# Performance work log

Measured on AMD Instinct MI355X. Metric: run time of the kernel, lower is better.

The kernel has to match this reference:

```python
import jax, jax.numpy as jnp
import numpy as np

N_NODES = 2_000_000
E = 1_000_000
MEM = 32      # memory_dim
MSG = 32      # message_dim
EMB = 32      # embed_dim
EDGE = 2      # edge_dim


def _linear_params(key, out_dim, in_dim):
    kw, kb = jax.random.split(key)
    bound = 1.0 / np.sqrt(in_dim)
    W = jax.random.uniform(kw, (out_dim, in_dim), jnp.float32, -bound, bound)
    b = jax.random.uniform(kb, (out_dim,), jnp.float32, -bound, bound)
    return W, b


def setup_inputs() -> dict:
    key = jax.random.key(0)
    ks = jax.random.split(key, 16)
    inp = {}
    inp["src_ids"] = jax.random.randint(ks[0], (E,), 0, N_NODES)
    inp["dst_ids"] = jax.random.randint(ks[1], (E,), 0, N_NODES)
    inp["edge_feat"] = jax.random.normal(ks[2], (E, EDGE), jnp.float32)
    inp["delta_t"] = jax.random.uniform(ks[3], (E, 1), jnp.float32)
    # persistent node memory (torch init is zeros; use randn for a non-trivial baseline)
    inp["memory"] = jax.random.normal(ks[4], (N_NODES, MEM), jnp.float32) * 0.1
    # MessageFunction MLP: (2*MEM + EDGE + 1) -> MSG -> MSG
    inp["msg_W1"], inp["msg_b1"] = _linear_params(ks[5], MSG, 2 * MEM + EDGE + 1)
    inp["msg_W2"], inp["msg_b2"] = _linear_params(ks[6], MSG, MSG)
    # GRUCell(MSG, MEM): weight_ih [3*MEM, MSG], weight_hh [3*MEM, MEM]
    inp["gru_w_ih"], inp["gru_b_ih"] = _linear_params(ks[7], 3 * MEM, MSG)
    inp["gru_w_hh"], inp["gru_b_hh"] = _linear_params(ks[8], 3 * MEM, MEM)
    # MultiheadAttention with seq_len=1: only V and out projections affect output
    inp["attn_Wv"], inp["attn_bv"] = _linear_params(ks[9], MEM, MEM)
    inp["attn_Wo"], inp["attn_bo"] = _linear_params(ks[10], MEM, MEM)
    # TemporalEmbedding MLP: (MEM + EDGE) -> EMB -> EMB
    inp["emb_W1"], inp["emb_b1"] = _linear_params(ks[11], EMB, MEM + EDGE)
    inp["emb_W2"], inp["emb_b2"] = _linear_params(ks[12], EMB, EMB)
    # AnomalyClassifier: EMB -> 32 -> 1
    inp["cls_W1"], inp["cls_b1"] = _linear_params(ks[13], 32, EMB)
    inp["cls_W2"], inp["cls_b2"] = _linear_params(ks[14], 1, 32)
    return inp


def reference(src_ids, dst_ids, edge_feat, delta_t, memory,
              msg_W1, msg_b1, msg_W2, msg_b2,
              gru_w_ih, gru_w_hh, gru_b_ih, gru_b_hh,
              attn_Wv, attn_bv, attn_Wo, attn_bo,
              emb_W1, emb_b1, emb_W2, emb_b2,
              cls_W1, cls_b1, cls_W2, cls_b2):
    # gather per-node memory  [E, MEM]
    src_mem = memory[src_ids]
    dst_mem = memory[dst_ids]

    # MessageFunction: concat + 2-layer MLP
    x = jnp.concatenate([src_mem, dst_mem, edge_feat, delta_t], axis=-1)  # [E, 67]
    h = jax.nn.relu(x @ msg_W1.T + msg_b1)
    msg = h @ msg_W2.T + msg_b2  # [E, MSG]

    # GRUCell update on dst memory (torch gate order: r, z, n)
    gi = msg @ gru_w_ih.T + gru_b_ih      # [E, 3*MEM]
    gh = dst_mem @ gru_w_hh.T + gru_b_hh  # [E, 3*MEM]
    i_r, i_z, i_n = jnp.split(gi, 3, axis=-1)
    h_r, h_z, h_n = jnp.split(gh, 3, axis=-1)
    r = jax.nn.sigmoid(i_r + h_r)
    z = jax.nn.sigmoid(i_z + h_z)
    n = jnp.tanh(i_n + r * h_n)
    updated = (1.0 - z) * n + z * dst_mem  # [E, MEM]
    # scatter back into persistent buffer (detached in the torch module)
    new_memory = memory.at[dst_ids].set(jax.lax.stop_gradient(updated))

    # TemporalEmbedding: self-attention over a length-1 sequence. softmax of a
    # single score is exactly 1, so attn_out == out_proj(v_proj(dst_mem)).
    attn_out = (dst_mem @ attn_Wv.T + attn_bv) @ attn_Wo.T + attn_bo  # [E, MEM]
    e = jnp.concatenate([attn_out, edge_feat], axis=-1)  # [E, MEM+EDGE]
    embed = jax.nn.relu(e @ emb_W1.T + emb_b1) @ emb_W2.T + emb_b2  # [E, EMB]

    # AnomalyClassifier (dropout is identity at eval)
    logits = jax.nn.relu(embed @ cls_W1.T + cls_b1) @ cls_W2.T + cls_b2  # [E, 1]
    probs = jax.nn.sigmoid(logits).squeeze(-1)  # [E]
    return probs, new_memory
```

## Files before the change

kernel.cpp:

```cpp
#include <hip/hip_runtime.h>
#include <hip/hip_bf16.h>

typedef float  f32x4v __attribute__((ext_vector_type(4)));
typedef short  bf16x8 __attribute__((ext_vector_type(8)));

#define NFRAG   26
#define TB_F32  512
#define FRG_U16 (NFRAG*512)
#define SHARE_BYTES (TB_F32*4 + FRG_U16*2)
#define SHARE_U4 (SHARE_BYTES/16)
#define WC_OFF 7168

#define BLK 256
#define COPY_BLOCKS 256
#define EDGE_BLOCKS 768
#define GRID (COPY_BLOCKS + EDGE_BLOCKS)
#define EDGE_WAVES (EDGE_BLOCKS * 4)

#define MFMA(a,b,c) __builtin_amdgcn_mfma_f32_16x16x32_bf16(a,b,c,0,0,0)

__device__ __forceinline__ float sigf(float v) { return 1.0f / (1.0f + __expf(-v)); }
__device__ __forceinline__ float tanhf_fast(float v) {
    float a = fabsf(v);
    float t = __expf(-2.0f * a);
    float r = (1.0f - t) / (1.0f + t);
    return v < 0.0f ? -r : r;
}
__device__ __forceinline__ unsigned pk(float a, float b) {
    union { __hip_bfloat162 h; unsigned u; } c;
    c.h = __float22bfloat162_rn(make_float2(a, b));
    return c.u;
}

union FragU { uint4 u4; bf16x8 s8; unsigned u[4]; };

__device__ __forceinline__ bf16x8 ldfrag(const unsigned short* frg, int idx_u16) {
    FragU c; c.u4 = *(const uint4*)(frg + idx_u16); return c.s8;
}
__device__ __forceinline__ f32x4v tbl(const float* tb, int idx_f32) {
    return *(const f32x4v*)(tb + idx_f32);
}
__device__ __forceinline__ bf16x8 relayout_reg(f32x4v h0, f32x4v h1) {
    FragU c;
    c.u[0] = pk(h0[0], h0[1]); c.u[1] = pk(h0[2], h0[3]);
    c.u[2] = pk(h1[0], h1[1]); c.u[3] = pk(h1[2], h1[3]);
    return c.s8;
}

__global__ void winner_k(const int* __restrict__ dst_ids, int* __restrict__ winner, int E) {
    int e = blockIdx.x * 256 + threadIdx.x;
    if (e < E) atomicMax(winner + dst_ids[e], e + 1);
}

__global__ void prep_k(const float* __restrict__ msg_W1, const float* __restrict__ msg_b1,
                       const float* __restrict__ msg_W2, const float* __restrict__ msg_b2,
                       const float* __restrict__ w_ih, const float* __restrict__ b_ih,
                       const float* __restrict__ w_hh, const float* __restrict__ b_hh,
                       const float* __restrict__ Wv, const float* __restrict__ bv,
                       const float* __restrict__ Wo, const float* __restrict__ bo,
                       const float* __restrict__ emb_W1, const float* __restrict__ emb_b1,
                       const float* __restrict__ emb_W2, const float* __restrict__ emb_b2,
                       const float* __restrict__ cls_W1, const float* __restrict__ cls_b1,
                       const float* __restrict__ cls_W2, float* __restrict__ WSf) {
    int t = threadIdx.x;
    float* tb = WSf;
    unsigned short* frg = (unsigned short*)(WSf + TB_F32);
    float* WC = WSf + WC_OFF;
    if (t < 32) {
        int j = t;
        tb[0*32+j]  = msg_b1[j];
        tb[1*32+j]  = msg_W1[j*67+64];
        tb[2*32+j]  = msg_W1[j*67+65];
        tb[3*32+j]  = msg_W1[j*67+66];
        tb[4*32+j]  = msg_b2[j];
        tb[5*32+j]  = b_ih[32+j] + b_hh[32+j];
        tb[6*32+j]  = b_ih[j] + b_hh[j];
        tb[7*32+j]  = b_hh[64+j];
        tb[8*32+j]  = b_ih[64+j];
        float a = bo[j];
        for (int o = 0; o < 32; ++o) a += Wo[j*32+o] * bv[o];
        tb[9*32+j]  = a;
        tb[10*32+j] = emb_b1[j];
        tb[11*32+j] = emb_W1[j*34+32];
        tb[12*32+j] = emb_W1[j*34+33];
        tb[13*32+j] = emb_b2[j];
        tb[14*32+j] = cls_b1[j];
        tb[15*32+j] = cls_W2[j];
    }
    for (int i = t; i < 1024; i += 256) {
        int j = i >> 5, k = i & 31;
        float a = 0.0f;
        for (int o = 0; o < 32; ++o) a += Wo[j*32+o] * Wv[o*32+k];
        WC[i] = a;
    }
    __syncthreads();
    for (int idx = t; idx < NFRAG * 512; idx += 256) {
        int f = idx >> 9, l = (idx >> 3) & 63, i = idx & 7;
        int r = l & 15, kb = ((l >> 4) << 3) + i;
        const float* P; int j0 = 0, k0 = 0, ld = 32;
        bool mapped = false;
        switch (f) {
            case 0:  P = msg_W1; j0 = 0;  k0 = 0;  ld = 67; break;
            case 1:  P = msg_W1; j0 = 0;  k0 = 32; ld = 67; break;
            case 2:  P = msg_W1; j0 = 16; k0 = 0;  ld = 67; break;
            case 3:  P = msg_W1; j0 = 16; k0 = 32; ld = 67; break;
            case 4:  P = msg_W2; j0 = 0;  mapped = true; break;
            case 5:  P = msg_W2; j0 = 16; mapped = true; break;
            case 6:  P = w_ih;   j0 = 32; mapped = true; break;
            case 7:  P = w_hh;   j0 = 32; break;
            case 8:  P = w_ih;   j0 = 48; mapped = true; break;
            case 9:  P = w_hh;   j0 = 48; break;
            case 10: P = w_ih;   j0 = 0;  mapped = true; break;
            case 11: P = w_hh;   j0 = 0;  break;
            case 12: P = w_ih;   j0 = 16; mapped = true; break;
            case 13: P = w_hh;   j0 = 16; break;
            case 14: P = w_hh;   j0 = 64; break;
            case 15: P = w_hh;   j0 = 80; break;
            case 16: P = w_ih;   j0 = 64; mapped = true; break;
            case 17: P = w_ih;   j0 = 80; mapped = true; break;
            case 18: P = WC;     j0 = 0;  break;
            case 19: P = WC;     j0 = 16; break;
            case 20: P = emb_W1; j0 = 0;  ld = 34; mapped = true; break;
            case 21: P = emb_W1; j0 = 16; ld = 34; mapped = true; break;
            case 22: P = emb_W2; j0 = 0;  mapped = true; break;
            case 23: P = emb_W2; j0 = 16; mapped = true; break;
            case 24: P = cls_W1; j0 = 0;  mapped = true; break;
            default: P = cls_W1; j0 = 16; mapped = true; break;
        }
        int kidx = kb;
        if (mapped) kidx = 16 * ((kb >> 2) & 1) + 4 * (kb >> 3) + (kb & 3);
        __hip_bfloat16 hv = __float2bfloat16(P[(j0 + r) * ld + k0 + kidx]);
        frg[idx] = *(unsigned short*)&hv;
    }
}

__device__ __forceinline__ void compute16(
    int grp, int E, int eI, int g, int lane,
    int e, int dst, int winv, float2 ef, float dtv,
    f32x4v sa, f32x4v sb, f32x4v da, f32x4v db, f32x4v t0, f32x4v t1,
    const float* tb, const unsigned short* frg, float clsb2,
    float* __restrict__ probs, float* __restrict__ out_mem) {
    int ob = 0, tbo = 0;
    asm volatile("" : "+v"(ob), "+v"(tbo));

    FragU Bs, Bd;
    Bs.u[0] = pk(sa[0], sa[1]); Bs.u[1] = pk(sa[2], sa[3]);
    Bs.u[2] = pk(sb[0], sb[1]); Bs.u[3] = pk(sb[2], sb[3]);
    Bd.u[0] = pk(da[0], da[1]); Bd.u[1] = pk(da[2], da[3]);
    Bd.u[2] = pk(db[0], db[1]); Bd.u[3] = pk(db[2], db[3]);
    f32x4v dmt[2]; dmt[0] = t0; dmt[1] = t1;

    f32x4v h[2];
#pragma unroll
    for (int jt = 0; jt < 2; ++jt) {
        f32x4v b1v = tbl(tb, 0*32 + jt*16 + 4*g + tbo);
        f32x4v w64 = tbl(tb, 1*32 + jt*16 + 4*g + tbo);
        f32x4v w65 = tbl(tb, 2*32 + jt*16 + 4*g + tbo);
        f32x4v w66 = tbl(tb, 3*32 + jt*16 + 4*g + tbo);
        f32x4v c;
#pragma unroll
        for (int i = 0; i < 4; ++i)
            c[i] = b1v[i] + ef.x * w64[i] + ef.y * w65[i] + dtv * w66[i];
        c = MFMA(ldfrag(frg, (jt*2+1)*512 + lane*8 + ob), Bd.s8, c);
        c = MFMA(ldfrag(frg, (jt*2+0)*512 + lane*8 + ob), Bs.s8, c);
#pragma unroll
        for (int i = 0; i < 4; ++i) c[i] = fmaxf(c[i], 0.0f);
        h[jt] = c;
    }
    bf16x8 Bh = relayout_reg(h[0], h[1]);

    f32x4v m[2];
#pragma unroll
    for (int jt = 0; jt < 2; ++jt)
        m[jt] = MFMA(ldfrag(frg, (4+jt)*512 + lane*8 + ob), Bh,
                     tbl(tb, 4*32 + jt*16 + 4*g + tbo));
    bf16x8 Bm = relayout_reg(m[0], m[1]);

    f32x4v zz[2], uu[2];
#pragma unroll
    for (int jt = 0; jt < 2; ++jt) {
        f32x4v c = tbl(tb, 5*32 + jt*16 + 4*g + tbo);
        c = MFMA(ldfrag(frg, (7+2*jt)*512 + lane*8 + ob), Bd.s8, c);
        c = MFMA(ldfrag(frg, (6+2*jt)*512 + lane*8 + ob), Bm, c);
#pragma unroll
        for (int i = 0; i < 4; ++i) c[i] = sigf(c[i]);
        zz[jt] = c;
    }
#pragma unroll
    for (int jt = 0; jt < 2; ++jt) {
        f32x4v c = tbl(tb, 6*32 + jt*16 + 4*g + tbo);
        c = MFMA(ldfrag(frg, (11+2*jt)*512 + lane*8 + ob), Bd.s8, c);
        c = MFMA(ldfrag(frg, (10+2*jt)*512 + lane*8 + ob), Bm, c);
        f32x4v hn = tbl(tb, 7*32 + jt*16 + 4*g + tbo);
        hn = MFMA(ldfrag(frg, (14+jt)*512 + lane*8 + ob), Bd.s8, hn);
        f32x4v bin = tbl(tb, 8*32 + jt*16 + 4*g + tbo);
        f32x4v npre;
#pragma unroll
        for (int i = 0; i < 4; ++i) npre[i] = fmaf(sigf(c[i]), hn[i], bin[i]);
        npre = MFMA(ldfrag(frg, (16+jt)*512 + lane*8 + ob), Bm, npre);
#pragma unroll
        for (int i = 0; i < 4; ++i) {
            float n = tanhf_fast(npre[i]);
            uu[jt][i] = n + zz[jt][i] * (dmt[jt][i] - n);
        }
    }
    if (winv == e + 1) {
        f32x4v* orow = (f32x4v*)(out_mem + (size_t)dst * 32);
        orow[g]     = uu[0];
        orow[4 + g] = uu[1];
    }

    f32x4v at[2];
#pragma unroll
    for (int jt = 0; jt < 2; ++jt)
        at[jt] = MFMA(ldfrag(frg, (18+jt)*512 + lane*8 + ob), Bd.s8,
                      tbl(tb, 9*32 + jt*16 + 4*g + tbo));
    bf16x8 Ba = relayout_reg(at[0], at[1]);
    f32x4v e1v[2];
#pragma unroll
    for (int jt = 0; jt < 2; ++jt) {
        f32x4v b  = tbl(tb, 10*32 + jt*16 + 4*g + tbo);
        f32x4v wa = tbl(tb, 11*32 + jt*16 + 4*g + tbo);
        f32x4v wb = tbl(tb, 12*32 + jt*16 + 4*g + tbo);
        f32x4v c;
#pragma unroll
        for (int i = 0; i < 4; ++i) c[i] = b[i] + ef.x * wa[i] + ef.y * wb[i];
        c = MFMA(ldfrag(frg, (20+jt)*512 + lane*8 + ob), Ba, c);
#pragma unroll
        for (int i = 0; i < 4; ++i) c[i] = fmaxf(c[i], 0.0f);
        e1v[jt] = c;
    }
    bf16x8 B1 = relayout_reg(e1v[0], e1v[1]);
    f32x4v e2v[2];
#pragma unroll
    for (int jt = 0; jt < 2; ++jt)
        e2v[jt] = MFMA(ldfrag(frg, (22+jt)*512 + lane*8 + ob), B1,
                       tbl(tb, 13*32 + jt*16 + 4*g + tbo));
    bf16x8 B2 = relayout_reg(e2v[0], e2v[1]);
    float part = 0.0f;
#pragma unroll
    for (int jt = 0; jt < 2; ++jt) {
        f32x4v c = MFMA(ldfrag(frg, (24+jt)*512 + lane*8 + ob), B2,
                        tbl(tb, 14*32 + jt*16 + 4*g + tbo));
        f32x4v w2 = tbl(tb, 15*32 + jt*16 + 4*g + tbo);
#pragma unroll
        for (int i = 0; i < 4; ++i) part = fmaf(fmaxf(c[i], 0.0f), w2[i], part);
    }
    part += __shfl_xor(part, 16);
    part += __shfl_xor(part, 32);
    if (lane < 16) {
        int ee = grp * 16 + eI;
        if (ee < E) probs[ee] = sigf(part + clsb2);
    }
}

__global__ __launch_bounds__(BLK, 4) void tgn_mfma16(
    const int* __restrict__ src_ids, const int* __restrict__ dst_ids,
    const float* __restrict__ edge_feat, const float* __restrict__ delta_t,
    const float* __restrict__ memory, const float* __restrict__ cls_b2,
    const float* __restrict__ WSf, const int* __restrict__ winner,
    float* __restrict__ probs, float* __restrict__ out_mem,
    int E, int N, int ngrp) {
    __shared__ uint4 sbuf[SHARE_U4];
    int bid = blockIdx.x, tid = threadIdx.x;

    if (bid < COPY_BLOCKS) {
        const f32x4v* m4 = (const f32x4v*)memory;
        f32x4v* o4 = (f32x4v*)out_mem;
        const long S = (long)COPY_BLOCKS * BLK;
        const long total4 = (long)N * 8;
        long i0 = (long)bid * BLK + tid;
        for (; i0 + 3 * S < total4; i0 += 4 * S) {
            long i1 = i0 + S, i2 = i0 + 2 * S, i3 = i0 + 3 * S;
            int w0 = winner[i0 >> 3];
            int w1 = winner[i1 >> 3];
            int w2 = winner[i2 >> 3];
            int w3 = winner[i3 >> 3];
            if (w0 == 0) o4[i0] = m4[i0];
            if (w1 == 0) o4[i1] = m4[i1];
            if (w2 == 0) o4[i2] = m4[i2];
            if (w3 == 0) o4[i3] = m4[i3];
        }
        for (; i0 < total4; i0 += S) {
            if (winner[i0 >> 3] == 0) o4[i0] = m4[i0];
        }
        return;
    }

    {
        const uint4* s = (const uint4*)WSf;
        for (int i = tid; i < SHARE_U4; i += BLK) sbuf[i] = s[i];
    }
    __syncthreads();
    const float* tb = (const float*)sbuf;
    const unsigned short* frg = (const unsigned short*)((const float*)sbuf + TB_F32);
    int wv = tid >> 6, lane = tid & 63;
    int eI = lane & 15, g = lane >> 4;
    int ewid = (bid - COPY_BLOCKS) * 4 + wv;
    float clsb2 = cls_b2[0];

#define PREF(P, G) do {                                                              \
    int ee = (G) * 16 + eI; if (ee >= E) ee = E - 1;                                 \
    e##P = ee;                                                                       \
    int sid = src_ids[ee]; dst##P = dst_ids[ee];                                     \
    ef##P = ((const float2*)edge_feat)[ee]; dt##P = delta_t[ee];                     \
    win##P = winner[dst##P];                                                         \
    const f32x4v* sp_ = (const f32x4v*)(memory + (size_t)sid * 32);                  \
    const f32x4v* dp_ = (const f32x4v*)(memory + (size_t)dst##P * 32);               \
    S##P##a = sp_[2*g]; S##P##b = sp_[2*g+1];                                        \
    D##P##a = dp_[2*g]; D##P##b = dp_[2*g+1];                                        \
    T##P##0 = dp_[g];   T##P##1 = dp_[4+g];                                          \
} while (0)

#define PIN(P) asm volatile("" : "+v"(S##P##a), "+v"(S##P##b), "+v"(D##P##a),        \
                                 "+v"(D##P##b), "+v"(T##P##0), "+v"(T##P##1),        \
                                 "+v"(win##P), "+v"(dt##P))

    int g0 = ewid;
    if (g0 < ngrp) {
        int eA, dstA, winA; float2 efA; float dtA;
        f32x4v SAa, SAb, DAa, DAb, TA0, TA1;
        int eB, dstB, winB; float2 efB; float dtB;
        f32x4v SBa, SBb, DBa, DBb, TB0, TB1;
        PREF(A, g0);
        for (;;) {
            int gn = g0 + EDGE_WAVES;
            { int gp = (gn < ngrp) ? gn : (ngrp - 1); PREF(B, gp); PIN(B); }
            compute16(g0, E, eI, g, lane, eA, dstA, winA, efA, dtA,
                      SAa, SAb, DAa, DAb, TA0, TA1,
                      tb, frg, clsb2, probs, out_mem);
            if (gn >= ngrp) break;
            g0 = gn;
            gn = g0 + EDGE_WAVES;
            { int gp = (gn < ngrp) ? gn : (ngrp - 1); PREF(A, gp); PIN(A); }
            compute16(g0, E, eI, g, lane, eB, dstB, winB, efB, dtB,
                      SBa, SBb, DBa, DBb, TB0, TB1,
                      tb, frg, clsb2, probs, out_mem);
            if (gn >= ngrp) break;
            g0 = gn;
        }
    }
#undef PREF
#undef PIN
}

extern "C" void kernel_launch(void* const* d_in, const int* in_sizes, int n_in,
                              void* d_out, int out_size, void* d_ws, size_t ws_size,
                              hipStream_t stream) {
    const int*   src_ids   = (const int*)d_in[0];
    const int*   dst_ids   = (const int*)d_in[1];
    const float* edge_feat = (const float*)d_in[2];
    const float* delta_t   = (const float*)d_in[3];
    const float* memory    = (const float*)d_in[4];
    const float* msg_W1 = (const float*)d_in[5],  *msg_b1 = (const float*)d_in[6];
    const float* msg_W2 = (const float*)d_in[7],  *msg_b2 = (const float*)d_in[8];
    const float* w_ih   = (const float*)d_in[9],  *b_ih   = (const float*)d_in[10];
    const float* w_hh   = (const float*)d_in[11], *b_hh   = (const float*)d_in[12];
    const float* Wv     = (const float*)d_in[13], *bv     = (const float*)d_in[14];
    const float* Wo     = (const float*)d_in[15], *bo     = (const float*)d_in[16];
    const float* emb_W1 = (const float*)d_in[17], *emb_b1 = (const float*)d_in[18];
    const float* emb_W2 = (const float*)d_in[19], *emb_b2 = (const float*)d_in[20];
    const float* cls_W1 = (const float*)d_in[21], *cls_b1 = (const float*)d_in[22];
    const float* cls_W2 = (const float*)d_in[23], *cls_b2 = (const float*)d_in[24];

    int E = in_sizes[0];
    int N = in_sizes[4] / 32;
    int ngrp = (E + 15) / 16;

    int*   winner = (int*)d_ws;
    float* WSf    = (float*)((char*)d_ws + (size_t)N * sizeof(int));
    float* probs  = (float*)d_out;
    float* outmem = probs + E;

    hipMemsetAsync(winner, 0, (size_t)N * sizeof(int), stream);
    winner_k<<<(E + 255) / 256, 256, 0, stream>>>(dst_ids, winner, E);
    prep_k<<<1, 256, 0, stream>>>(msg_W1, msg_b1, msg_W2, msg_b2,
                                  w_ih, b_ih, w_hh, b_hh,
                                  Wv, bv, Wo, bo,
                                  emb_W1, emb_b1, emb_W2, emb_b2,
                                  cls_W1, cls_b1, cls_W2, WSf);
    tgn_mfma16<<<GRID, BLK, 0, stream>>>(src_ids, dst_ids, edge_feat, delta_t,
                                         memory, cls_b2, WSf, winner,
                                         probs, outmem, E, N, ngrp);
}
```

Measured before the change: 293.8 us.

## Software-pipeline edge gathers with inline-asm loads and branchless trash-buffer stores

Restructures the edge loop into a two-deep software pipeline. Edge ids and features for the next-next group are issued with inline-asm global loads, and the gathered memory rows for the next group are issued before the current group's compute. Explicit s_waitcnt vmcnt(3) points with sched barriers keep the compiler from serialising these loads, so gather latency can be hidden behind MFMA work. The conditional memory-row store is made branchless: losing edges write to a per-wave trash area in the workspace, which removes divergence but adds extra stores. Manual vmcnt accounting is fragile, because stores also count against vmcnt and the loads are opaque to the compiler.

```diff
diff --git a/kernel.cpp b/kernel.cpp
--- a/kernel.cpp
+++ b/kernel.cpp
@@ -2,6 +2,7 @@
 #include <hip/hip_bf16.h>
 
 typedef float  f32x4v __attribute__((ext_vector_type(4)));
+typedef float  f32x2v __attribute__((ext_vector_type(2)));
 typedef short  bf16x8 __attribute__((ext_vector_type(8)));
 
 #define NFRAG   26
@@ -136,10 +137,10 @@
 
 __device__ __forceinline__ void compute16(
     int grp, int E, int eI, int g, int lane,
-    int e, int dst, int winv, float2 ef, float dtv,
+    int e, int dst, int winv, f32x2v ef, float dtv,
     f32x4v sa, f32x4v sb, f32x4v da, f32x4v db, f32x4v t0, f32x4v t1,
     const float* tb, const unsigned short* frg, float clsb2,
-    float* __restrict__ probs, float* __restrict__ out_mem) {
+    float* __restrict__ probs, float* __restrict__ out_mem, float* trash) {
     int ob = 0, tbo = 0;
     asm volatile("" : "+v"(ob), "+v"(tbo));
 
@@ -160,7 +161,7 @@
         f32x4v c;
 #pragma unroll
         for (int i = 0; i < 4; ++i)
-            c[i] = b1v[i] + ef.x * w64[i] + ef.y * w65[i] + dtv * w66[i];
+            c[i] = b1v[i] + ef[0] * w64[i] + ef[1] * w65[i] + dtv * w66[i];
         c = MFMA(ldfrag(frg, (jt*2+1)*512 + lane*8 + ob), Bd.s8, c);
         c = MFMA(ldfrag(frg, (jt*2+0)*512 + lane*8 + ob), Bs.s8, c);
 #pragma unroll
@@ -204,10 +205,14 @@
             uu[jt][i] = n + zz[jt][i] * (dmt[jt][i] - n);
         }
     }
-    if (winv == e + 1) {
+    {
+        bool w = (winv == e + 1);
         f32x4v* orow = (f32x4v*)(out_mem + (size_t)dst * 32);
-        orow[g]     = uu[0];
-        orow[4 + g] = uu[1];
+        f32x4v* tr   = (f32x4v*)trash;
+        f32x4v* p0 = w ? orow + g     : tr + g;
+        f32x4v* p1 = w ? orow + 4 + g : tr + 4 + g;
+        *p0 = uu[0];
+        *p1 = uu[1];
     }
 
     f32x4v at[2];
@@ -224,7 +229,7 @@
         f32x4v wb = tbl(tb, 12*32 + jt*16 + 4*g + tbo);
         f32x4v c;
 #pragma unroll
-        for (int i = 0; i < 4; ++i) c[i] = b[i] + ef.x * wa[i] + ef.y * wb[i];
+        for (int i = 0; i < 4; ++i) c[i] = b[i] + ef[0] * wa[i] + ef[1] * wb[i];
         c = MFMA(ldfrag(frg, (20+jt)*512 + lane*8 + ob), Ba, c);
 #pragma unroll
         for (int i = 0; i < 4; ++i) c[i] = fmaxf(c[i], 0.0f);
@@ -259,7 +264,7 @@
     const float* __restrict__ edge_feat, const float* __restrict__ delta_t,
     const float* __restrict__ memory, const float* __restrict__ cls_b2,
     const float* __restrict__ WSf, const int* __restrict__ winner,
-    float* __restrict__ probs, float* __restrict__ out_mem,
+    float* __restrict__ probs, float* __restrict__ out_mem, float* trashbase,
     int E, int N, int ngrp) {
     __shared__ uint4 sbuf[SHARE_U4];
     int bid = blockIdx.x, tid = threadIdx.x;
@@ -298,50 +303,100 @@
     int eI = lane & 15, g = lane >> 4;
     int ewid = (bid - COPY_BLOCKS) * 4 + wv;
     float clsb2 = cls_b2[0];
-
-#define PREF(P, G) do {                                                              \
-    int ee = (G) * 16 + eI; if (ee >= E) ee = E - 1;                                 \
-    e##P = ee;                                                                       \
-    int sid = src_ids[ee]; dst##P = dst_ids[ee];                                     \
-    ef##P = ((const float2*)edge_feat)[ee]; dt##P = delta_t[ee];                     \
-    win##P = winner[dst##P];                                                         \
-    const f32x4v* sp_ = (const f32x4v*)(memory + (size_t)sid * 32);                  \
-    const f32x4v* dp_ = (const f32x4v*)(memory + (size_t)dst##P * 32);               \
-    S##P##a = sp_[2*g]; S##P##b = sp_[2*g+1];                                        \
-    D##P##a = dp_[2*g]; D##P##b = dp_[2*g+1];                                        \
-    T##P##0 = dp_[g];   T##P##1 = dp_[4+g];                                          \
+    float* trash = trashbase + (((bid - COPY_BLOCKS) * 4 + wv) & 31) * 32;
+
+#define IDS_ASM(P, G) do {                                                           \
+    int ee_ = (G) * 16 + eI; if (ee_ >= E) ee_ = E - 1;                              \
+    e##P = ee_;                                                                      \
+    asm volatile("global_load_dword %0, %1, off"                                     \
+                 : "=v"(sid##P) : "v"((unsigned long long)(src_ids + ee_)));         \
+    asm volatile("global_load_dword %0, %1, off"                                     \
+                 : "=v"(dst##P) : "v"((unsigned long long)(dst_ids + ee_)));         \
+    asm volatile("global_load_dwordx2 %0, %1, off"                                   \
+                 : "=v"(ef##P) : "v"((unsigned long long)(edge_feat + 2*(size_t)ee_)));\
+    asm volatile("global_load_dword %0, %1, off"                                     \
+                 : "=v"(dt##P) : "v"((unsigned long long)(delta_t + ee_)));          \
 } while (0)
 
-#define PIN(P) asm volatile("" : "+v"(S##P##a), "+v"(S##P##b), "+v"(D##P##a),        \
-                                 "+v"(D##P##b), "+v"(T##P##0), "+v"(T##P##1),        \
-                                 "+v"(win##P), "+v"(dt##P))
-
-    int g0 = ewid;
-    if (g0 < ngrp) {
-        int eA, dstA, winA; float2 efA; float dtA;
+#define ROWS_ASM(P) do {                                                             \
+    unsigned long long sb_ = (unsigned long long)(memory + (size_t)sid##P * 32);     \
+    unsigned long long db_ = (unsigned long long)(memory + (size_t)dst##P * 32);     \
+    asm volatile("global_load_dwordx4 %0, %1, off" : "=v"(S##P##a) : "v"(sb_ + 32ull*g));      \
+    asm volatile("global_load_dwordx4 %0, %1, off" : "=v"(S##P##b) : "v"(sb_ + 32ull*g + 16)); \
+    asm volatile("global_load_dwordx4 %0, %1, off" : "=v"(D##P##a) : "v"(db_ + 32ull*g));      \
+    asm volatile("global_load_dwordx4 %0, %1, off" : "=v"(D##P##b) : "v"(db_ + 32ull*g + 16)); \
+    asm volatile("global_load_dwordx4 %0, %1, off" : "=v"(T##P##0) : "v"(db_ + 16ull*g));      \
+    asm volatile("global_load_dwordx4 %0, %1, off" : "=v"(T##P##1) : "v"(db_ + 64 + 16ull*g)); \
+    asm volatile("global_load_dword %0, %1, off"                                     \
+                 : "=v"(win##P) : "v"((unsigned long long)(winner + dst##P)));       \
+} while (0)
+
+#define WAITPF(Q, P) do {                                                            \
+    asm volatile("s_waitcnt vmcnt(3)"                                                \
+        : "+v"(S##Q##a), "+v"(S##Q##b), "+v"(D##Q##a), "+v"(D##Q##b),                \
+          "+v"(T##Q##0), "+v"(T##Q##1), "+v"(win##Q),                                \
+          "+v"(sid##P), "+v"(dst##P), "+v"(ef##P), "+v"(dt##P) :: "memory");         \
+    __builtin_amdgcn_sched_barrier(0);                                               \
+} while (0)
+
+    int gA = ewid, gB = ewid + EDGE_WAVES;
+    if (gA < ngrp) {
+        int eA, sidA, dstA, winA; f32x2v efA; float dtA;
         f32x4v SAa, SAb, DAa, DAb, TA0, TA1;
-        int eB, dstB, winB; float2 efB; float dtB;
+        int eB, sidB, dstB, winB; f32x2v efB; float dtB;
         f32x4v SBa, SBb, DBa, DBb, TB0, TB1;
-        PREF(A, g0);
+
+        {
+            int ee = gA * 16 + eI; if (ee >= E) ee = E - 1;
+            eA = ee;
+            sidA = src_ids[ee]; dstA = dst_ids[ee];
+            efA = ((const f32x2v*)edge_feat)[ee]; dtA = delta_t[ee];
+            winA = winner[dstA];
+            const f32x4v* sp_ = (const f32x4v*)memory + (size_t)sidA * 8;
+            const f32x4v* dp_ = (const f32x4v*)memory + (size_t)dstA * 8;
+            SAa = sp_[2*g]; SAb = sp_[2*g+1];
+            DAa = dp_[2*g]; DAb = dp_[2*g+1];
+            TA0 = dp_[g];   TA1 = dp_[4+g];
+            int gp = (gB < ngrp) ? gB : (ngrp - 1);
+            int ee2 = gp * 16 + eI; if (ee2 >= E) ee2 = E - 1;
+            eB = ee2;
+            sidB = src_ids[ee2]; dstB = dst_ids[ee2];
+            efB = ((const f32x2v*)edge_feat)[ee2]; dtB = delta_t[ee2];
+        }
+
         for (;;) {
-            int gn = g0 + EDGE_WAVES;
-            { int gp = (gn < ngrp) ? gn : (ngrp - 1); PREF(B, gp); PIN(B); }
-            compute16(g0, E, eI, g, lane, eA, dstA, winA, efA, dtA,
-                      SAa, SAb, DAa, DAb, TA0, TA1,
-                      tb, frg, clsb2, probs, out_mem);
-            if (gn >= ngrp) break;
-            g0 = gn;
-            gn = g0 + EDGE_WAVES;
-            { int gp = (gn < ngrp) ? gn : (ngrp - 1); PREF(A, gp); PIN(A); }
-            compute16(g0, E, eI, g, lane, eB, dstB, winB, efB, dtB,
-                      SBa, SBb, DBa, DBb, TB0, TB1,
-                      tb, frg, clsb2, probs, out_mem);
-            if (gn >= ngrp) break;
-            g0 = gn;
-        }
-    }
-#undef PREF
-#undef PIN
+            ROWS_ASM(B);
+            int gnA = gA + 2 * EDGE_WAVES;
+            {
+                int ce = eA, cd = dstA; f32x2v cef = efA; float cdt = dtA;
+                int gp = (gnA < ngrp) ? gnA : (ngrp - 1);
+                IDS_ASM(A, gp);
+                compute16(gA, E, eI, g, lane, ce, cd, winA, cef, cdt,
+                          SAa, SAb, DAa, DAb, TA0, TA1,
+                          tb, frg, clsb2, probs, out_mem, trash);
+            }
+            if (gB >= ngrp) break;
+            WAITPF(B, A);
+
+            ROWS_ASM(A);
+            int gnB = gB + 2 * EDGE_WAVES;
+            {
+                int ce = eB, cd = dstB; f32x2v cef = efB; float cdt = dtB;
+                int gp = (gnB < ngrp) ? gnB : (ngrp - 1);
+                IDS_ASM(B, gp);
+                compute16(gB, E, eI, g, lane, ce, cd, winB, cef, cdt,
+                          SBa, SBb, DBa, DBb, TB0, TB1,
+                          tb, frg, clsb2, probs, out_mem, trash);
+            }
+            gA = gnA;
+            if (gA >= ngrp) break;
+            WAITPF(A, B);
+            gB = gnB;
+        }
+    }
+#undef IDS_ASM
+#undef ROWS_ASM
+#undef WAITPF
 }
 
 extern "C" void kernel_launch(void* const* d_in, const int* in_sizes, int n_in,
@@ -371,6 +426,7 @@
     float* WSf    = (float*)((char*)d_ws + (size_t)N * sizeof(int));
     float* probs  = (float*)d_out;
     float* outmem = probs + E;
+    float* trash  = WSf + WC_OFF;
 
     hipMemsetAsync(winner, 0, (size_t)N * sizeof(int), stream);
     winner_k<<<(E + 255) / 256, 256, 0, stream>>>(dst_ids, winner, E);
@@ -381,5 +437,5 @@
                                   cls_W1, cls_b1, cls_W2, WSf);
     tgn_mfma16<<<GRID, BLK, 0, stream>>>(src_ids, dst_ids, edge_feat, delta_t,
                                          memory, cls_b2, WSf, winner,
-                                         probs, outmem, E, N, ngrp);
-}
+                                         probs, outmem, trash, E, N, ngrp);
+}
```

Result: no change. 292.5 us (-0.4%).
